# Optimization experiments

Measured on AMD Instinct MI355X. Metric: run time of the kernel, lower is better.

The kernel has to match this reference:

```python
import jax, jax.numpy as jnp
import numpy as np

NS, NV = 32, 8                      # scalar / vector multiplicities
N_NODES, N_EDGES, N_EF = 10000, 100000, 64
W1, W2, W3, W4 = NS*NS, NV*NV, NS*NV, NV*NS   # path weight sizes
WNUM = W1 + W2 + W3 + W4            # 1600
D_NODE = NS + 3*NV                  # 56

def mish(x):
    return x * jnp.tanh(jax.nn.softplus(x))

def setup_inputs() -> dict:
    key = jax.random.key(0)
    ks = jax.random.split(key, 8)
    return dict(
        node_attr=jax.random.normal(ks[0], (N_NODES, D_NODE), jnp.float32),
        edge_index=jax.random.randint(ks[1], (2, N_EDGES), 0, N_NODES),
        edge_attr=jax.random.normal(ks[2], (N_EDGES, N_EF), jnp.float32),
        edge_sh=jax.random.normal(ks[3], (N_EDGES, 4), jnp.float32),
        fc1_w=jax.random.normal(ks[4], (N_EF, N_EF), jnp.float32) / np.sqrt(N_EF),
        fc1_b=jnp.zeros((N_EF,), jnp.float32),
        fc2_w=jax.random.normal(ks[5], (N_EF, WNUM), jnp.float32) / np.sqrt(N_EF),
        fc2_b=jnp.zeros((WNUM,), jnp.float32),
        bn_gamma_s=jnp.ones((NS,), jnp.float32),
        bn_beta_s=jnp.zeros((NS,), jnp.float32),
        bn_gamma_v=jnp.ones((NV,), jnp.float32),
    )

def reference(node_attr, edge_index, edge_attr, edge_sh,
              fc1_w, fc1_b, fc2_w, fc2_b,
              bn_gamma_s, bn_beta_s, bn_gamma_v):
    edge_src, edge_dst = edge_index[0], edge_index[1]
    # edge-conditioned TP weights: Linear -> Mish -> Linear
    w = mish(edge_attr @ fc1_w + fc1_b) @ fc2_w + fc2_b            # [E, WNUM]
    w1 = w[:, :W1].reshape(-1, NS, NS)           # 0e x 0e -> 0e
    w2 = w[:, W1:W1+W2].reshape(-1, NV, NV)      # 1o x 0e -> 1o
    w3 = w[:, W1+W2:W1+W2+W3].reshape(-1, NS, NV)  # 0e x 1o -> 1o
    w4 = w[:, W1+W2+W3:].reshape(-1, NV, NS)     # 1o x 1o -> 0e
    # gather destination node features
    x = node_attr[edge_dst]
    s = x[:, :NS]                                # [E,NS]
    v = x[:, NS:].reshape(-1, NV, 3)             # [E,NV,3]
    sh0 = edge_sh[:, 0]                          # [E]
    sh1 = edge_sh[:, 1:4]                        # [E,3]
    # path normalization: 1/sqrt(total fan-in per output irrep) = 1/sqrt(NS+NV)
    a = 1.0 / np.sqrt(float(NS + NV))
    dot = jnp.einsum('euc,ec->eu', v, sh1) / np.sqrt(3.0)  # CG(1,1,0)
    out_s = a * (jnp.einsum('eu,euw->ew', s * sh0[:, None], w1)
               + jnp.einsum('eu,euw->ew', dot, w4))          # [E,NS]
    out_v = a * (jnp.einsum('euc,euw->ewc', v * sh0[:, None, None], w2)
               + jnp.einsum('eu,ec,euw->ewc', s, sh1, w3))   # [E,NV,3]
    tp = jnp.concatenate([out_s, out_v.reshape(-1, 3*NV)], axis=-1)  # [E,D_NODE]
    # scatter-mean over edge_src
    summ = jax.ops.segment_sum(tp, edge_src, num_segments=N_NODES)
    cnt = jax.ops.segment_sum(jnp.ones((N_EDGES,), tp.dtype), edge_src, num_segments=N_NODES)
    out = summ / jnp.maximum(cnt, 1.0)[:, None]
    # residual (in/out irreps equal -> pad is a no-op)
    out = out + node_attr
    # e3nn-style BatchNorm (training batch stats), eps=1e-4, component norm
    eps = 1e-4
    os = out[:, :NS]
    ov = out[:, NS:].reshape(-1, NV, 3)
    mu = os.mean(axis=0)
    osc = os - mu
    var = (osc * osc).mean(axis=0)
    os_n = osc * jax.lax.rsqrt(var + eps) * bn_gamma_s + bn_beta_s
    vn = (ov * ov).mean(axis=-1).mean(axis=0)                 # [NV]
    ov_n = ov * (jax.lax.rsqrt(vn + eps) * bn_gamma_v)[None, :, None]
    return jnp.concatenate([os_n, ov_n.reshape(-1, 3*NV)], axis=-1)
```

## Files before the change

kernel.cpp:

```cpp
#include <hip/hip_runtime.h>
#include <stdint.h>

#define NNODES 10000
#define NEDGES 100000
#define DNODE 56
#define JTOT 1600
#define EBLK 782
#define TBLK 400

typedef __attribute__((ext_vector_type(8))) short short8;
typedef __attribute__((ext_vector_type(4))) float floatx4;
typedef __attribute__((ext_vector_type(16))) float floatx16;

__device__ __forceinline__ unsigned short f2bf(float f) {
  unsigned u = __float_as_uint(f);
  u = u + 0x7fffu + ((u >> 16) & 1u);
  return (unsigned short)(u >> 16);
}
__device__ __forceinline__ float bf2f(unsigned short u) {
  return __uint_as_float(((unsigned)u) << 16);
}

__device__ __forceinline__ float mishf(float x) {
  float e = __expf(x);
  float z = 1.f + e; z = z * z;
  float t = (z - 1.f) / (z + 1.f);
  t = (x > 40.f) ? 1.f : t;
  return x * t;
}

__device__ __forceinline__ void async_ld16(void* lds, const void* gp) {
  __builtin_amdgcn_global_load_lds(
      (const __attribute__((address_space(1))) unsigned int*)gp,
      (__attribute__((address_space(3))) unsigned int*)lds, 16, 0, 0);
}

__global__ __launch_bounds__(256, 4) void k_hidtr(const float* __restrict__ ea,
                                                  const float* __restrict__ fc1w,
                                                  const float* __restrict__ fc1b,
                                                  const float* __restrict__ fc2w,
                                                  const int* __restrict__ eidx,
                                                  int* __restrict__ cntn,
                                                  unsigned short* __restrict__ hb,
                                                  unsigned short* __restrict__ G) {
  const int bid = blockIdx.x, tid = threadIdx.x;

  if (bid >= EBLK) {
    int idx = (bid - EBLK) * 256 + tid;
    if (idx < 64 * JTOT) {
      int jt = idx >> 11;
      int r  = idx & 2047;
      int s  = r >> 9;
      int l  = (r >> 3) & 63;
      int i  = r & 7;
      int j  = jt * 32 + (l & 31);
      int k  = s * 16 + (l >> 5) * 8 + i;
      G[idx] = f2bf(fc2w[k * JTOT + j]);
    }
    return;
  }

  __shared__ unsigned short T[64 * 72];
  __shared__ unsigned short E[128 * 72];
  __shared__ float b1s[64];
  const int e0 = bid * 128;
  if (tid < 128) {
    int e = e0 + tid;
    if (e < NEDGES) atomicAdd(&cntn[eidx[e]], 1);
  }
  if (tid < 64) b1s[tid] = fc1b[tid];
  #pragma unroll
  for (int it = 0; it < 4; it++) {
    int q = tid + 256 * it;
    int k = q >> 4, j4 = (q & 15) * 4;
    float4 v = *(const float4*)(fc1w + (size_t)q * 4);
    T[(j4+0)*72 + k] = f2bf(v.x);
    T[(j4+1)*72 + k] = f2bf(v.y);
    T[(j4+2)*72 + k] = f2bf(v.z);
    T[(j4+3)*72 + k] = f2bf(v.w);
  }
  #pragma unroll
  for (int it = 0; it < 8; it++) {
    int q = tid + 256 * it;
    int e = q >> 4, k4 = (q & 15) * 4;
    int ge = e0 + e;
    float4 v = (ge < NEDGES) ? *(const float4*)(ea + (size_t)ge * 64 + k4)
                             : make_float4(0.f, 0.f, 0.f, 0.f);
    ushort4 p;
    p.x = f2bf(v.x); p.y = f2bf(v.y); p.z = f2bf(v.z); p.w = f2bf(v.w);
    *(ushort4*)(&E[e*72 + k4]) = p;
  }
  __syncthreads();

  const int wave = tid >> 6, lane = tid & 63, col = lane & 15, rg = lane >> 4;
  short8 bf[2][2];
  #pragma unroll
  for (int nt = 0; nt < 2; nt++) {
    int er = wave*32 + nt*16 + col;
    bf[nt][0] = *(const short8*)(&E[er*72 + rg*8]);
    bf[nt][1] = *(const short8*)(&E[er*72 + 32 + rg*8]);
  }
  floatx4 acc[4][2];
  #pragma unroll
  for (int jt = 0; jt < 4; jt++) {
    int j = jt*16 + col;
    short8 a0 = *(const short8*)(&T[j*72 + rg*8]);
    short8 a1 = *(const short8*)(&T[j*72 + 32 + rg*8]);
    float4 bb = *(const float4*)(&b1s[jt*16 + rg*4]);
    #pragma unroll
    for (int nt = 0; nt < 2; nt++) {
      floatx4 c = {bb.x, bb.y, bb.z, bb.w};
      c = __builtin_amdgcn_mfma_f32_16x16x32_bf16(a0, bf[nt][0], c, 0, 0, 0);
      c = __builtin_amdgcn_mfma_f32_16x16x32_bf16(a1, bf[nt][1], c, 0, 0, 0);
      acc[jt][nt] = c;
    }
  }
  #pragma unroll
  for (int jt = 0; jt < 4; jt++)
    #pragma unroll
    for (int nt = 0; nt < 2; nt++) {
      ushort4 p;
      p.x = f2bf(mishf(acc[jt][nt][0]));
      p.y = f2bf(mishf(acc[jt][nt][1]));
      p.z = f2bf(mishf(acc[jt][nt][2]));
      p.w = f2bf(mishf(acc[jt][nt][3]));
      *(ushort4*)(&E[(wave*32 + nt*16 + col)*72 + jt*16 + rg*4]) = p;
    }
  #pragma unroll
  for (int it = 0; it < 4; it++) {
    int g = it*64 + lane;
    int r = g >> 3, c = g & 7;
    int ge = e0 + wave*32 + r;
    if (ge < NEDGES) {
      short8 v = *(const short8*)(&E[(wave*32 + r)*72 + c*8]);
      *(short8*)(hb + (size_t)ge*64 + c*8) = v;
    }
  }
}

__global__ __launch_bounds__(1024) void k_scan(const int* __restrict__ cntn,
                                               int* __restrict__ offs,
                                               int* __restrict__ cursor,
                                               int* __restrict__ gdone) {
  __shared__ int ts[1024];
  int t = threadIdx.x;
  if (t == 0) gdone[0] = 0;
  int base = t * 10;
  int loc[10]; int s = 0;
  #pragma unroll
  for (int i = 0; i < 10; i++) {
    int idx = base + i;
    int v = (idx < NNODES) ? cntn[idx] : 0;
    loc[i] = s; s += v;
  }
  ts[t] = s;
  __syncthreads();
  for (int off = 1; off < 1024; off <<= 1) {
    int v = (t >= off) ? ts[t - off] : 0;
    __syncthreads();
    ts[t] += v;
    __syncthreads();
  }
  int excl = (t == 0) ? 0 : ts[t - 1];
  #pragma unroll
  for (int i = 0; i < 10; i++) {
    int idx = base + i;
    if (idx < NNODES) { int o = excl + loc[i]; offs[idx] = o; cursor[idx] = o; }
  }
  if (t == 1023) offs[NNODES] = ts[1023];
}

__global__ __launch_bounds__(256, 4) void k_tp(
    const unsigned short* __restrict__ hb,
    const unsigned short* __restrict__ G,
    const float* __restrict__ fc2b,
    const int* __restrict__ eidx,
    const float* __restrict__ node_attr,
    const float* __restrict__ edge_sh,
    int* __restrict__ cursor,
    float* __restrict__ tp) {
  __shared__ short Gs[2][4096];
  __shared__ unsigned short wls[4][2048];
  __shared__ float b2s[JTOT];
  __shared__ int pos_s[4][32];
  const int tid = threadIdx.x;
  const int wave = tid >> 6, lane = tid & 63;
  for (int i = tid; i < JTOT; i += 256) b2s[i] = fc2b[i];

  const int e0w = blockIdx.x * 128 + wave * 32;
  unsigned short* Wt = &wls[wave][0];
  {
    int el = lane & 31, hh = lane >> 5;
    int e = e0w + el;
    bool valid = e < NEDGES;
    int dst = valid ? eidx[NEDGES + e] : 0;
    const float* na = node_attr + (size_t)dst * DNODE;
    if (hh == 0) {
      pos_s[wave][el] = valid ? atomicAdd(&cursor[eidx[e]], 1) : 0;
      #pragma unroll
      for (int u = 0; u < 32; u += 4) {
        float4 v = valid ? *(const float4*)(na + u) : make_float4(0.f,0.f,0.f,0.f);
        Wt[(u+0)*32 + el] = f2bf(v.x);
        Wt[(u+1)*32 + el] = f2bf(v.y);
        Wt[(u+2)*32 + el] = f2bf(v.z);
        Wt[(u+3)*32 + el] = f2bf(v.w);
      }
    } else {
      float4 sh = valid ? *(const float4*)(edge_sh + 4*(size_t)e) : make_float4(0.f,0.f,0.f,0.f);
      const float rs3 = 0.57735026918962576f;
      #pragma unroll
      for (int u = 0; u < 8; u++) {
        float v0 = valid ? na[32 + u*3 + 0] : 0.f;
        float v1 = valid ? na[32 + u*3 + 1] : 0.f;
        float v2 = valid ? na[32 + u*3 + 2] : 0.f;
        Wt[(32 + u*3 + 0)*32 + el] = f2bf(v0);
        Wt[(32 + u*3 + 1)*32 + el] = f2bf(v1);
        Wt[(32 + u*3 + 2)*32 + el] = f2bf(v2);
        Wt[(56 + u)*32 + el] = f2bf((v0*sh.y + v1*sh.z + v2*sh.w) * rs3);
      }
    }
  }

  const int col = lane & 31, h = lane >> 5;
  const int e = e0w + col;
  const bool vld = e < NEDGES;
  float sh0c, sh1c[3];
  short8 bfr[4];
  const short8 zfrag = {0,0,0,0,0,0,0,0};
  if (vld) {
    float4 sh = *(const float4*)(edge_sh + 4*(size_t)e);
    sh0c = sh.x; sh1c[0] = sh.y; sh1c[1] = sh.z; sh1c[2] = sh.w;
    const unsigned short* hp = hb + (size_t)e * 64;
    #pragma unroll
    for (int s = 0; s < 4; s++)
      bfr[s] = *(const short8*)(hp + s*16 + h*8);
  } else {
    sh0c = 0.f; sh1c[0] = sh1c[1] = sh1c[2] = 0.f;
    #pragma unroll
    for (int s = 0; s < 4; s++) bfr[s] = zfrag;
  }

  float sacc[16], vacc[12];
  #pragma unroll
  for (int i = 0; i < 16; i++) sacc[i] = 0.f;
  #pragma unroll
  for (int i = 0; i < 12; i++) vacc[i] = 0.f;

  auto stage = [&](int ch, int b) {
    const unsigned short* gsrc = G + (size_t)ch * 4096 + tid * 8;
    #pragma unroll
    for (int i = 0; i < 2; i++)
      async_ld16(&Gs[b][(i*256 + wave*64) * 8], gsrc + i*256*8);
  };

  int buf = 0;
  auto gemm_tile = [&](int jt, int t) -> floatx16 {
    const short* gb = &Gs[buf][t * 2048];
    short8 a0 = *(const short8*)(gb + lane*8);
    short8 a1 = *(const short8*)(gb + 512 + lane*8);
    short8 a2 = *(const short8*)(gb + 1024 + lane*8);
    short8 a3 = *(const short8*)(gb + 1536 + lane*8);
    floatx16 C;
    #pragma unroll
    for (int q = 0; q < 4; q++) {
      float4 b = *(const float4*)&b2s[jt*32 + 8*q + 4*h];
      C[q*4+0] = b.x; C[q*4+1] = b.y; C[q*4+2] = b.z; C[q*4+3] = b.w;
    }
    C = __builtin_amdgcn_mfma_f32_32x32x16_bf16(a0, bfr[0], C, 0, 0, 0);
    C = __builtin_amdgcn_mfma_f32_32x32x16_bf16(a1, bfr[1], C, 0, 0, 0);
    C = __builtin_amdgcn_mfma_f32_32x32x16_bf16(a2, bfr[2], C, 0, 0, 0);
    C = __builtin_amdgcn_mfma_f32_32x32x16_bf16(a3, bfr[3], C, 0, 0, 0);
    return C;
  };
  auto apply_s = [&](const floatx16& C, float cf) {
    #pragma unroll
    for (int i = 0; i < 16; i++) sacc[i] = fmaf(cf, C[i], sacc[i]);
  };
  auto apply_w2 = [&](const floatx16& C, int ubase) {
    #pragma unroll
    for (int q = 0; q < 4; q++) {
      const int u = ubase + q;
      #pragma unroll
      for (int c = 0; c < 3; c++) {
        float cf = bf2f(Wt[(32 + u*3 + c)*32 + col]) * sh0c;
        #pragma unroll
        for (int r = 0; r < 4; r++)
          vacc[c*4+r] = fmaf(cf, C[q*4+r], vacc[c*4+r]);
      }
    }
  };
  auto apply_w3 = [&](const floatx16& C, int ubase) {
    #pragma unroll
    for (int q = 0; q < 4; q++) {
      float sv = bf2f(Wt[(ubase + q)*32 + col]);
      #pragma unroll
      for (int c = 0; c < 3; c++) {
        float cf = sv * sh1c[c];
        #pragma unroll
        for (int r = 0; r < 4; r++)
          vacc[c*4+r] = fmaf(cf, C[q*4+r], vacc[c*4+r]);
      }
    }
  };

  const int cc0 = blockIdx.x % 25;
  stage(cc0, 0);
  __syncthreads();

  #pragma unroll 1
  for (int cc = 0; cc < 25; cc++) {
    int c = cc0 + cc; if (c >= 25) c -= 25;
    if (cc < 24) { int cn = c + 1; if (cn >= 25) cn = 0; stage(cn, buf ^ 1); }
    const int jt0 = c * 2;
    if (jt0 < 32) {
      floatx16 C0 = gemm_tile(jt0, 0);
      apply_s(C0, bf2f(Wt[jt0*32 + col]) * sh0c);
      floatx16 C1 = gemm_tile(jt0 + 1, 1);
      apply_s(C1, bf2f(Wt[(jt0+1)*32 + col]) * sh0c);
    } else if (jt0 == 32) {
      floatx16 C0 = gemm_tile(32, 0);
      apply_w2(C0, 0);
      floatx16 C1 = gemm_tile(33, 1);
      apply_w2(C1, 4);
    } else if (jt0 < 42) {
      floatx16 C0 = gemm_tile(jt0, 0);
      apply_w3(C0, (jt0 - 34) * 4);
      floatx16 C1 = gemm_tile(jt0 + 1, 1);
      apply_w3(C1, (jt0 - 33) * 4);
    } else {
      floatx16 C0 = gemm_tile(jt0, 0);
      apply_s(C0, bf2f(Wt[(56 + jt0 - 42)*32 + col]));
      floatx16 C1 = gemm_tile(jt0 + 1, 1);
      apply_s(C1, bf2f(Wt[(56 + jt0 - 41)*32 + col]));
    }
    buf ^= 1;
    __syncthreads();
  }

  const float ascale = 0.15811388300841897f;
  if (vld) {
    float* rowp = tp + (size_t)pos_s[wave][col] * DNODE;
    #pragma unroll
    for (int q = 0; q < 4; q++) {
      float4 v = make_float4(ascale*sacc[q*4+0], ascale*sacc[q*4+1],
                             ascale*sacc[q*4+2], ascale*sacc[q*4+3]);
      *(float4*)(rowp + 8*q + 4*h) = v;
    }
    float tmp[12];
    #pragma unroll
    for (int r = 0; r < 4; r++)
      #pragma unroll
      for (int c = 0; c < 3; c++) tmp[r*3 + c] = ascale * vacc[c*4 + r];
    #pragma unroll
    for (int j = 0; j < 3; j++)
      *(float4*)(rowp + 32 + 12*h + j*4) = *(float4*)&tmp[j*4];
  }
}

__global__ __launch_bounds__(256) void k_gather(const float* __restrict__ tp,
                                                const int* __restrict__ offs,
                                                const float* __restrict__ node_attr,
                                                float* __restrict__ pre,
                                                float* __restrict__ pstat,
                                                int* __restrict__ gdone,
                                                float* __restrict__ stats) {
  __shared__ float redS[4*64], redQ[4*64];
  __shared__ int amLast;
  int t = threadIdx.x, wave = t >> 6, lane = t & 63;
  int gw = blockIdx.x * 4 + wave;
  const int W = 640 * 4;
  int off = (lane < DNODE) ? lane : 0;
  float ssum = 0.f, ssq = 0.f;
  for (int n = gw; n < NNODES; n += W) {
    int beg = offs[n], end = offs[n+1];
    float acc = 0.f;
    int i = beg;
    for (; i + 4 <= end; i += 4) {
      float v0 = tp[(size_t)(i+0)*DNODE + off];
      float v1 = tp[(size_t)(i+1)*DNODE + off];
      float v2 = tp[(size_t)(i+2)*DNODE + off];
      float v3 = tp[(size_t)(i+3)*DNODE + off];
      acc += (v0 + v1) + (v2 + v3);
    }
    for (; i < end; i++) acc += tp[(size_t)i*DNODE + off];
    int c = end - beg; if (c < 1) c = 1;
    float m = acc / (float)c + node_attr[(size_t)n*DNODE + off];
    if (lane < DNODE) { pre[(size_t)n*DNODE + lane] = m; ssum += m; ssq += m*m; }
  }
  redS[wave*64 + lane] = ssum;
  redQ[wave*64 + lane] = ssq;
  __syncthreads();
  if (wave == 0 && lane < DNODE) {
    float a = redS[lane] + redS[64+lane] + redS[128+lane] + redS[192+lane];
    float b = redQ[lane] + redQ[64+lane] + redQ[128+lane] + redQ[192+lane];
    pstat[(size_t)blockIdx.x*112 + lane] = a;
    pstat[(size_t)blockIdx.x*112 + 56 + lane] = b;
  }
  __syncthreads();
  if (t == 0) {
    __threadfence();
    amLast = (atomicAdd(gdone, 1) == 639) ? 1 : 0;
  }
  __syncthreads();
  if (amLast) {
    __threadfence();
    int f = t & 127, hh = t >> 7;
    float v = 0.f;
    if (f < 112) {
      #pragma unroll 8
      for (int b = hh; b < 640; b += 2) v += pstat[(size_t)b*112 + f];
      redS[hh*128 + f] = v;
    }
    __syncthreads();
    if (t < 112) stats[t] = redS[t] + redS[128 + t];
  }
}

__global__ __launch_bounds__(256) void k_norm(const float* __restrict__ pre,
                                              const float* __restrict__ stats,
                                              const float* __restrict__ gs,
                                              const float* __restrict__ bs,
                                              const float* __restrict__ gv,
                                              float* __restrict__ out) {
  int idx = blockIdx.x * 256 + threadIdx.x;
  if (idx >= NNODES * DNODE) return;
  int n = idx / DNODE;
  int d = idx - n * DNODE;
  float val = pre[idx];
  const float invN = 1.f / (float)NNODES;
  float res;
  if (d < 32) {
    float mu = stats[d] * invN;
    float var = stats[56 + d] * invN - mu * mu;
    res = (val - mu) * rsqrtf(var + 1e-4f) * gs[d] + bs[d];
  } else {
    int wi = (d - 32) / 3;
    float vn = (stats[56 + 32 + wi*3] + stats[56 + 32 + wi*3 + 1] +
                stats[56 + 32 + wi*3 + 2]) * (invN / 3.f);
    res = val * rsqrtf(vn + 1e-4f) * gv[wi];
  }
  out[idx] = res;
}

extern "C" void kernel_launch(void* const* d_in, const int* in_sizes, int n_in,
                              void* d_out, int out_size, void* d_ws, size_t ws_size,
                              hipStream_t stream) {
  const float* node_attr = (const float*)d_in[0];
  const int*   eidx      = (const int*)d_in[1];
  const float* edge_attr = (const float*)d_in[2];
  const float* edge_sh   = (const float*)d_in[3];
  const float* fc1w      = (const float*)d_in[4];
  const float* fc1b      = (const float*)d_in[5];
  const float* fc2w      = (const float*)d_in[6];
  const float* fc2b      = (const float*)d_in[7];
  const float* gs        = (const float*)d_in[8];
  const float* bs        = (const float*)d_in[9];
  const float* gv        = (const float*)d_in[10];

  float* ws = (float*)d_ws;
  float* tp    = ws;
  float* pre   = ws + 5600000;
  float* stats = ws + 6160000;
  float* pstat = ws + 6160128;
  int*   cntn  = (int*)(ws + 6231808);
  int*   offs  = (int*)(ws + 6241808);
  int*   cursor= (int*)(ws + 6251816);
  int*   gdone = (int*)(ws + 6261816);
  unsigned short* G  = (unsigned short*)(ws + 6261824);
  unsigned short* hb = (unsigned short*)(ws + 6313024);

  hipMemsetAsync(cntn, 0, (size_t)10000 * 4, stream);
  k_hidtr<<<EBLK + TBLK, 256, 0, stream>>>(edge_attr, fc1w, fc1b, fc2w, eidx, cntn, hb, G);
  k_scan<<<1, 1024, 0, stream>>>(cntn, offs, cursor, gdone);
  k_tp<<<782, 256, 0, stream>>>(hb, G, fc2b, eidx, node_attr, edge_sh, cursor, tp);
  k_gather<<<640, 256, 0, stream>>>(tp, offs, node_attr, pre, pstat, gdone, stats);
  k_norm<<<(NNODES * DNODE + 255) / 256, 256, 0, stream>>>(pre, stats, gs, bs, gv, (float*)d_out);
}
```

Baseline: 226.0 us.

## Fuse batchnorm into gather kernel via grid-wide flag barrier

Removes the separate normalization kernel and folds it into the gather kernel. The last block to finish reduces the statistics, then sets a flag that all other blocks spin on, and each block normalizes the nodes it produced. This saves a kernel launch and a pass over the tensor, at the cost of a software grid barrier, which needs all 640 blocks to be resident at once or it deadlocks. It also lowers the k_tp launch-bounds occupancy hint from 4 to 3 blocks per CU.

```diff
diff --git a/kernel.cpp b/kernel.cpp
--- a/kernel.cpp
+++ b/kernel.cpp
@@ -7,6 +7,7 @@
 #define JTOT 1600
 #define EBLK 782
 #define TBLK 400
+#define GBLK 640
 
 typedef __attribute__((ext_vector_type(8))) short short8;
 typedef __attribute__((ext_vector_type(4))) float floatx4;
@@ -141,10 +142,10 @@
 __global__ __launch_bounds__(1024) void k_scan(const int* __restrict__ cntn,
                                                int* __restrict__ offs,
                                                int* __restrict__ cursor,
-                                               int* __restrict__ gdone) {
+                                               int* __restrict__ sync2) {
   __shared__ int ts[1024];
   int t = threadIdx.x;
-  if (t == 0) gdone[0] = 0;
+  if (t < 2) sync2[t] = 0;
   int base = t * 10;
   int loc[10]; int s = 0;
   #pragma unroll
@@ -170,7 +171,7 @@
   if (t == 1023) offs[NNODES] = ts[1023];
 }
 
-__global__ __launch_bounds__(256, 4) void k_tp(
+__global__ __launch_bounds__(256, 3) void k_tp(
     const unsigned short* __restrict__ hb,
     const unsigned short* __restrict__ G,
     const float* __restrict__ fc2b,
@@ -362,13 +363,17 @@
                                                 const float* __restrict__ node_attr,
                                                 float* __restrict__ pre,
                                                 float* __restrict__ pstat,
-                                                int* __restrict__ gdone,
-                                                float* __restrict__ stats) {
+                                                int* __restrict__ sync2,
+                                                float* __restrict__ stats,
+                                                const float* __restrict__ gs,
+                                                const float* __restrict__ bs,
+                                                const float* __restrict__ gv,
+                                                float* __restrict__ out) {
   __shared__ float redS[4*64], redQ[4*64];
   __shared__ int amLast;
   int t = threadIdx.x, wave = t >> 6, lane = t & 63;
   int gw = blockIdx.x * 4 + wave;
-  const int W = 640 * 4;
+  const int W = GBLK * 4;
   int off = (lane < DNODE) ? lane : 0;
   float ssum = 0.f, ssq = 0.f;
   for (int n = gw; n < NNODES; n += W) {
@@ -399,7 +404,7 @@
   __syncthreads();
   if (t == 0) {
     __threadfence();
-    amLast = (atomicAdd(gdone, 1) == 639) ? 1 : 0;
+    amLast = (atomicAdd(&sync2[0], 1) == GBLK - 1) ? 1 : 0;
   }
   __syncthreads();
   if (amLast) {
@@ -408,38 +413,38 @@
     float v = 0.f;
     if (f < 112) {
       #pragma unroll 8
-      for (int b = hh; b < 640; b += 2) v += pstat[(size_t)b*112 + f];
+      for (int b = hh; b < GBLK; b += 2) v += pstat[(size_t)b*112 + f];
       redS[hh*128 + f] = v;
     }
     __syncthreads();
     if (t < 112) stats[t] = redS[t] + redS[128 + t];
-  }
-}
-
-__global__ __launch_bounds__(256) void k_norm(const float* __restrict__ pre,
-                                              const float* __restrict__ stats,
-                                              const float* __restrict__ gs,
-                                              const float* __restrict__ bs,
-                                              const float* __restrict__ gv,
-                                              float* __restrict__ out) {
-  int idx = blockIdx.x * 256 + threadIdx.x;
-  if (idx >= NNODES * DNODE) return;
-  int n = idx / DNODE;
-  int d = idx - n * DNODE;
-  float val = pre[idx];
+    __threadfence();
+    __syncthreads();
+    if (t == 0) atomicExch(&sync2[1], 1);
+  }
+  if (t == 0) {
+    while (atomicAdd(&sync2[1], 0) == 0) __builtin_amdgcn_s_sleep(8);
+  }
+  __syncthreads();
+  __threadfence();
   const float invN = 1.f / (float)NNODES;
-  float res;
-  if (d < 32) {
-    float mu = stats[d] * invN;
-    float var = stats[56 + d] * invN - mu * mu;
-    res = (val - mu) * rsqrtf(var + 1e-4f) * gs[d] + bs[d];
-  } else {
-    int wi = (d - 32) / 3;
+  float mu_l = 0.f, sc_l = 0.f, ad_l = 0.f;
+  if (lane < 32) {
+    float mu = stats[lane] * invN;
+    float var = stats[56 + lane] * invN - mu * mu;
+    mu_l = mu; sc_l = rsqrtf(var + 1e-4f) * gs[lane]; ad_l = bs[lane];
+  } else if (lane < DNODE) {
+    int wi = (lane - 32) / 3;
     float vn = (stats[56 + 32 + wi*3] + stats[56 + 32 + wi*3 + 1] +
                 stats[56 + 32 + wi*3 + 2]) * (invN / 3.f);
-    res = val * rsqrtf(vn + 1e-4f) * gv[wi];
-  }
-  out[idx] = res;
+    sc_l = rsqrtf(vn + 1e-4f) * gv[wi];
+  }
+  for (int n = gw; n < NNODES; n += W) {
+    if (lane < DNODE) {
+      float val = pre[(size_t)n*DNODE + lane];
+      out[(size_t)n*DNODE + lane] = (val - mu_l) * sc_l + ad_l;
+    }
+  }
 }
 
 extern "C" void kernel_launch(void* const* d_in, const int* in_sizes, int n_in,
@@ -465,14 +470,14 @@
   int*   cntn  = (int*)(ws + 6231808);
   int*   offs  = (int*)(ws + 6241808);
   int*   cursor= (int*)(ws + 6251816);
-  int*   gdone = (int*)(ws + 6261816);
+  int*   sync2 = (int*)(ws + 6261816);
   unsigned short* G  = (unsigned short*)(ws + 6261824);
   unsigned short* hb = (unsigned short*)(ws + 6313024);
 
   hipMemsetAsync(cntn, 0, (size_t)10000 * 4, stream);
   k_hidtr<<<EBLK + TBLK, 256, 0, stream>>>(edge_attr, fc1w, fc1b, fc2w, eidx, cntn, hb, G);
-  k_scan<<<1, 1024, 0, stream>>>(cntn, offs, cursor, gdone);
+  k_scan<<<1, 1024, 0, stream>>>(cntn, offs, cursor, sync2);
   k_tp<<<782, 256, 0, stream>>>(hb, G, fc2b, eidx, node_attr, edge_sh, cursor, tp);
-  k_gather<<<640, 256, 0, stream>>>(tp, offs, node_attr, pre, pstat, gdone, stats);
-  k_norm<<<(NNODES * DNODE + 255) / 256, 256, 0, stream>>>(pre, stats, gs, bs, gv, (float*)d_out);
-}
+  k_gather<<<GBLK, 256, 0, stream>>>(tp, offs, node_attr, pre, pstat, sync2, stats,
+                                     gs, bs, gv, (float*)d_out);
+}
```

Measured after the change: 296.9 us. 31.4% more time.
